# Kernel tuning notes

Hardware: AMD Instinct MI355X
Metric: run time of the kernel (lower is better)

The kernel has to match this reference:

```python
import jax, jax.numpy as jnp
import numpy as np


def setup_inputs() -> dict:
    key = jax.random.key(0)
    k1, k2 = jax.random.split(key)
    E, T, N = 65536, 4096, 10000
    edge_index = jax.random.randint(k1, (2, E), 0, N)
    # target edges are a subset of edge_index columns so every target exists
    target_edges = edge_index[:, :T]
    score = jax.random.normal(k2, (E,), dtype=jnp.float32)
    return {
        "edge_index": edge_index,
        "score": score,
        "target_edges": target_edges,
        "num_nodes": N,
    }


def reference(edge_index, score, target_edges, num_nodes):
    # Vectorized form of the per-target-edge loop:
    # for each target edge (s, d):
    #   mask_e      = (src_e == s) | (dst_e == d)
    #   CE over score[mask] with target = position of the exact edge (s, d)
    #   contribution = CE / K  where K = mask.sum()
    src, dst = edge_index[0], edge_index[1]            # [E]
    t_src, t_dst = target_edges[0], target_edges[1]    # [T]

    same_src = src[None, :] == t_src[:, None]          # [T, E]
    same_dst = dst[None, :] == t_dst[:, None]          # [T, E]
    mask = same_src | same_dst                         # candidate set per target
    is_tgt = same_src & same_dst                       # exact target edge hits

    exists = jnp.any(is_tgt, axis=1)                   # [T]
    K = jnp.sum(mask, axis=1).astype(score.dtype)      # [T] ragged subset sizes

    NEG = jnp.asarray(-1e30, score.dtype)
    masked_logits = jnp.where(mask, score[None, :], NEG)   # [T, E]
    lse = jax.nn.logsumexp(masked_logits, axis=1)           # [T]

    # argmax over bool picks the FIRST matching edge, matching torch argmax(-1)
    tgt_idx = jnp.argmax(is_tgt, axis=1)                # [T]
    tgt_logit = score[tgt_idx]                          # [T]

    # cross_entropy = lse - target_logit; divided by subset size K
    loss_t = jnp.where(exists, (lse - tgt_logit) / K, 0.0)
    return jnp.sum(loss_t) / target_edges.shape[1]
```

## Files before the change

### kernel.cpp

```cpp
#include <hip/hip_runtime.h>
#include <hip/hip_bf16.h>
#include <stdint.h>


#define HLOG 13
#define HSZ  (1u << HLOG)
#define NCAP 16384
#define EMPTY64 0xFFFFFFFFFFFFFFFFull
#define M40     ((1ull << 40) - 1)
#define CNT1    (1ull << 40)
#define FSCALE      4194304.0f
#define INV_FSCALE  (1.0f / 4194304.0f)

typedef unsigned long long u64;
typedef unsigned int u32;

__device__ __forceinline__ u32 hash64(u64 k) {
    return (u32)((k * 0x9E3779B97F4A7C15ull) >> (64 - HLOG));
}

__global__ __launch_bounds__(256) void la_insert(
    const int* __restrict__ tsrc, const int* __restrict__ tdst,
    u64* __restrict__ hkey, int T)
{
    const int t = blockIdx.x * 256 + threadIdx.x;
    if (t >= T) return;
    const u64 key = ((u64)(u32)tsrc[t] << 32) | (u32)tdst[t];
    u32 h = hash64(key);
    while (true) {
        const u64 prev = atomicCAS(&hkey[h], EMPTY64, key);
        if (prev == EMPTY64 || prev == key) break;
        h = (h + 1) & (HSZ - 1);
    }
}

__global__ __launch_bounds__(256) void la_edges(
    const int* __restrict__ src, const int* __restrict__ dst,
    const float* __restrict__ score,
    const u64* __restrict__ hkey, u64* __restrict__ hpack,
    u32* __restrict__ hmin,
    u64* __restrict__ nodeS, u64* __restrict__ nodeD, int E)
{
    const int e = blockIdx.x * 256 + threadIdx.x;
    if (e >= E) return;
    const int s = src[e], d = dst[e];
    const float ev = __expf(score[e]);
    const u64 add = (u64)(ev * FSCALE + 0.5f) + CNT1;

    atomicAdd(&nodeS[s], add);
    atomicAdd(&nodeD[d], add);

    const u64 key = ((u64)(u32)s << 32) | (u32)d;
    u32 h = hash64(key);
    while (true) {
        const u64 k2 = hkey[h];
        if (k2 == EMPTY64) break;
        if (k2 == key) {
            atomicAdd(&hpack[h], add);
            atomicMin(&hmin[h], (u32)e);
            break;
        }
        h = (h + 1) & (HSZ - 1);
    }
}

__global__ __launch_bounds__(64) void la_targets(
    const int* __restrict__ tsrc, const int* __restrict__ tdst,
    const float* __restrict__ score,
    const u64* __restrict__ hkey, const u64* __restrict__ hpack,
    const u32* __restrict__ hmin,
    const u64* __restrict__ nodeS, const u64* __restrict__ nodeD,
    float* __restrict__ partial, int T)
{
    const int t = blockIdx.x * 64 + threadIdx.x;
    float local = 0.0f;
    if (t < T) {
        const int a = tsrc[t], b = tdst[t];
        const u64 key = ((u64)(u32)a << 32) | (u32)b;
        u32 h = hash64(key);
        int slot = -1;
        while (true) {
            const u64 k2 = hkey[h];
            if (k2 == key) { slot = (int)h; break; }
            if (k2 == EMPTY64) break;
            h = (h + 1) & (HSZ - 1);
        }
        if (slot >= 0) {
            const u64 pk = hpack[slot];
            const u64 cb = pk >> 40;
            if (cb > 0) {
                const u64 pa = nodeS[a], pb = nodeD[b];
                const u64 Sfix = (pa & M40) + (pb & M40) - (pk & M40);
                const u64 Kc   = (pa >> 40) + (pb >> 40) - cb;
                const float S  = (float)Sfix * INV_FSCALE;
                local = (logf(S) - score[hmin[slot]]) / (float)Kc;
            }
        }
    }
    for (int off = 32; off > 0; off >>= 1) local += __shfl_down(local, off);
    if (threadIdx.x == 0) partial[blockIdx.x] = local;
}

__global__ __launch_bounds__(64) void la_final(
    const float* __restrict__ partial, float* __restrict__ out, int nb, int T)
{
    float s = 0.0f;
    for (int i = threadIdx.x; i < nb; i += 64) s += partial[i];
    for (int off = 32; off > 0; off >>= 1) s += __shfl_down(s, off);
    if (threadIdx.x == 0) out[0] = s / (float)T;
}

#define NT   8
#define BLK  256

__global__ __launch_bounds__(BLK) void la_loss_main(
    const int* __restrict__ src, const int* __restrict__ dst,
    const float* __restrict__ score,
    const int* __restrict__ tsrc, const int* __restrict__ tdst,
    float* __restrict__ partial, int E, int T)
{
    const int tid   = threadIdx.x;
    const int tbase = blockIdx.x * NT;
    if (tbase >= T) return;

    int ts[NT], td[NT];
#pragma unroll
    for (int j = 0; j < NT; ++j) {
        int tj = tbase + j; if (tj > T - 1) tj = T - 1;
        ts[j] = tsrc[tj];
        td[j] = tdst[tj];
    }

    float S[NT]; float Kc[NT]; int idx[NT];
#pragma unroll
    for (int j = 0; j < NT; ++j) { S[j] = 0.0f; Kc[j] = 0.0f; idx[j] = 0x7fffffff; }

    for (int it = tid * 4; it < E; it += BLK * 4) {
        const int4   vs = *reinterpret_cast<const int4*>(src + it);
        const int4   vd = *reinterpret_cast<const int4*>(dst + it);
        const float4 sc = *reinterpret_cast<const float4*>(score + it);
        const int   es[4] = { vs.x, vs.y, vs.z, vs.w };
        const int   ed[4] = { vd.x, vd.y, vd.z, vd.w };
        const float ev[4] = { __expf(sc.x), __expf(sc.y), __expf(sc.z), __expf(sc.w) };
#pragma unroll
        for (int j = 0; j < NT; ++j) {
#pragma unroll
            for (int k = 0; k < 4; ++k) {
                const bool ms = (es[k] == ts[j]);
                const bool md = (ed[k] == td[j]);
                const bool m  = ms | md;
                S[j]  += m ? ev[k] : 0.0f;
                Kc[j] += m ? 1.0f  : 0.0f;
                idx[j] = (ms & md) ? min(idx[j], it + k) : idx[j];
            }
        }
    }

#pragma unroll
    for (int j = 0; j < NT; ++j) {
        for (int off = 32; off > 0; off >>= 1) {
            S[j]  += __shfl_down(S[j],  off);
            Kc[j] += __shfl_down(Kc[j], off);
            idx[j] = min(idx[j], __shfl_down(idx[j], off));
        }
    }

    __shared__ float sS[4][NT];
    __shared__ float sK[4][NT];
    __shared__ int   sI[4][NT];
    const int wave = tid >> 6;
    const int lane = tid & 63;
    if (lane == 0) {
#pragma unroll
        for (int j = 0; j < NT; ++j) { sS[wave][j] = S[j]; sK[wave][j] = Kc[j]; sI[wave][j] = idx[j]; }
    }
    __syncthreads();

    if (tid < NT && (tbase + tid) < T) {
        float Ssum = 0.0f, Ksum = 0.0f;
        int im = 0x7fffffff;
#pragma unroll
        for (int w = 0; w < 4; ++w) {
            Ssum += sS[w][tid]; Ksum += sK[w][tid]; im = min(im, sI[w][tid]);
        }
        float loss = 0.0f;
        if (im != 0x7fffffff) loss = (logf(Ssum) - score[im]) / Ksum;
        partial[tbase + tid] = loss;
    }
}

__global__ __launch_bounds__(256) void la_loss_reduce(
    const float* __restrict__ partial, float* __restrict__ out, int T)
{
    float s = 0.0f;
    for (int i = threadIdx.x; i < T; i += 256) s += partial[i];
    for (int off = 32; off > 0; off >>= 1) s += __shfl_down(s, off);
    __shared__ float acc[4];
    if ((threadIdx.x & 63) == 0) acc[threadIdx.x >> 6] = s;
    __syncthreads();
    if (threadIdx.x == 0) out[0] = (acc[0] + acc[1] + acc[2] + acc[3]) / (float)T;
}


extern "C" void kernel_launch(void* const* d_in, const int* in_sizes, int n_in,
                              void* d_out, int out_size, void* d_ws, size_t ws_size,
                              hipStream_t stream) {
    const int*   edge_index = (const int*)d_in[0];
    const float* score      = (const float*)d_in[1];
    const int*   target     = (const int*)d_in[2];

    const int E = in_sizes[0] / 2;
    const int T = in_sizes[2] / 2;

    const int* src  = edge_index;
    const int* dst  = edge_index + E;
    const int* tsrc = target;
    const int* tdst = target + T;

    const size_t HKEY_B  = (size_t)HSZ * 8;
    const size_t HMIN_B  = (size_t)HSZ * 4;
    const size_t HPACK_B = (size_t)HSZ * 8;
    const size_t NODE_B  = (size_t)NCAP * 8;
    const int    nb3     = (T + 63) / 64;
    const size_t need = HKEY_B + HMIN_B + HPACK_B + 2 * NODE_B + (size_t)nb3 * 4;

    if (ws_size >= need) {
        uint8_t* p = (uint8_t*)d_ws;
        u64* hkey    = (u64*)p;                 p += HKEY_B;
        u32* hmin    = (u32*)p;                 p += HMIN_B;
        u64* hpack   = (u64*)p;                 p += HPACK_B;
        u64* nodeS   = (u64*)p;                 p += NODE_B;
        u64* nodeD   = (u64*)p;                 p += NODE_B;
        float* partial = (float*)p;

        hipMemsetAsync(hkey,  0xFF, HKEY_B + HMIN_B, stream);
        hipMemsetAsync(hpack, 0x00, HPACK_B + 2 * NODE_B, stream);

        la_insert<<<(T + 255) / 256, 256, 0, stream>>>(tsrc, tdst, hkey, T);
        la_edges<<<(E + 255) / 256, 256, 0, stream>>>(src, dst, score, hkey,
                                                      hpack, hmin, nodeS, nodeD, E);
        la_targets<<<nb3, 64, 0, stream>>>(tsrc, tdst, score, hkey, hpack, hmin,
                                           nodeS, nodeD, partial, T);
        la_final<<<1, 64, 0, stream>>>(partial, (float*)d_out, nb3, T);
    } else {
        float* partial = (float*)d_ws;
        la_loss_main<<<(T + NT - 1) / NT, BLK, 0, stream>>>(src, dst, score,
                                                            tsrc, tdst, partial, E, T);
        la_loss_reduce<<<1, 256, 0, stream>>>(partial, (float*)d_out, T);
    }
}
```

Before: 36.43 us.

## Filter edges by target-node bitmaps and fuse init and final reduction kernels

Replaces the two memsets with a single init kernel, and builds source/destination bitmaps of target nodes during hash insertion. The edge pass uses these bitmaps to skip atomics and hash probes for edges that touch no target node. The final reduction is folded into the targets kernel through a last-block-done counter with release/acquire atomics. This cuts launch count and atomic traffic, at the cost of extra bitmap atomics and a dependence on node ids being below NCAP.

```diff
diff --git a/kernel.cpp b/kernel.cpp
--- a/kernel.cpp
+++ b/kernel.cpp
@@ -6,6 +6,7 @@
 #define HLOG 13
 #define HSZ  (1u << HLOG)
 #define NCAP 16384
+#define NBW  (NCAP / 32)
 #define EMPTY64 0xFFFFFFFFFFFFFFFFull
 #define M40     ((1ull << 40) - 1)
 #define CNT1    (1ull << 40)
@@ -19,13 +20,29 @@
     return (u32)((k * 0x9E3779B97F4A7C15ull) >> (64 - HLOG));
 }
 
+#define FF_BYTES   ((size_t)HSZ * 8 + (size_t)HSZ * 4)
+#define Z_BYTES    ((size_t)HSZ * 8 + 2 * (size_t)NCAP * 8 + 2 * (size_t)NBW * 4 + 8)
+
+__global__ __launch_bounds__(256) void la_init(u64* __restrict__ p,
+                                               int n_ff, int n_tot)
+{
+    int i = blockIdx.x * 256 + threadIdx.x;
+    const int stride = gridDim.x * 256;
+    for (; i < n_tot; i += stride)
+        p[i] = (i < n_ff) ? EMPTY64 : 0ull;
+}
+
 __global__ __launch_bounds__(256) void la_insert(
     const int* __restrict__ tsrc, const int* __restrict__ tdst,
-    u64* __restrict__ hkey, int T)
+    u64* __restrict__ hkey, u32* __restrict__ sbit, u32* __restrict__ dbit,
+    int T)
 {
     const int t = blockIdx.x * 256 + threadIdx.x;
     if (t >= T) return;
-    const u64 key = ((u64)(u32)tsrc[t] << 32) | (u32)tdst[t];
+    const u32 a = (u32)tsrc[t], b = (u32)tdst[t];
+    if (a < NCAP) atomicOr(&sbit[a >> 5], 1u << (a & 31));
+    if (b < NCAP) atomicOr(&dbit[b >> 5], 1u << (b & 31));
+    const u64 key = ((u64)a << 32) | b;
     u32 h = hash64(key);
     while (true) {
         const u64 prev = atomicCAS(&hkey[h], EMPTY64, key);
@@ -39,28 +56,37 @@
     const float* __restrict__ score,
     const u64* __restrict__ hkey, u64* __restrict__ hpack,
     u32* __restrict__ hmin,
-    u64* __restrict__ nodeS, u64* __restrict__ nodeD, int E)
+    u64* __restrict__ nodeS, u64* __restrict__ nodeD,
+    const u32* __restrict__ sbit, const u32* __restrict__ dbit, int E)
 {
     const int e = blockIdx.x * 256 + threadIdx.x;
     if (e >= E) return;
-    const int s = src[e], d = dst[e];
+    const u32 s = (u32)src[e], d = (u32)dst[e];
+    if (s >= NCAP || d >= NCAP) return;
+
+    const bool hs = (sbit[s >> 5] >> (s & 31)) & 1u;
+    const bool hd = (dbit[d >> 5] >> (d & 31)) & 1u;
+    if (!hs && !hd) return;
+
     const float ev = __expf(score[e]);
     const u64 add = (u64)(ev * FSCALE + 0.5f) + CNT1;
 
-    atomicAdd(&nodeS[s], add);
-    atomicAdd(&nodeD[d], add);
-
-    const u64 key = ((u64)(u32)s << 32) | (u32)d;
-    u32 h = hash64(key);
-    while (true) {
-        const u64 k2 = hkey[h];
-        if (k2 == EMPTY64) break;
-        if (k2 == key) {
-            atomicAdd(&hpack[h], add);
-            atomicMin(&hmin[h], (u32)e);
-            break;
-        }
-        h = (h + 1) & (HSZ - 1);
+    if (hs) atomicAdd(&nodeS[s], add);
+    if (hd) atomicAdd(&nodeD[d], add);
+
+    if (hs && hd) {
+        const u64 key = ((u64)s << 32) | d;
+        u32 h = hash64(key);
+        while (true) {
+            const u64 k2 = hkey[h];
+            if (k2 == EMPTY64) break;
+            if (k2 == key) {
+                atomicAdd(&hpack[h], add);
+                atomicMin(&hmin[h], (u32)e);
+                break;
+            }
+            h = (h + 1) & (HSZ - 1);
+        }
     }
 }
 
@@ -70,13 +96,15 @@
     const u64* __restrict__ hkey, const u64* __restrict__ hpack,
     const u32* __restrict__ hmin,
     const u64* __restrict__ nodeS, const u64* __restrict__ nodeD,
-    float* __restrict__ partial, int T)
-{
-    const int t = blockIdx.x * 64 + threadIdx.x;
+    float* __restrict__ partial, u32* __restrict__ done,
+    float* __restrict__ out, int T)
+{
+    const int nb = gridDim.x;
+    const int t  = blockIdx.x * 64 + threadIdx.x;
     float local = 0.0f;
     if (t < T) {
-        const int a = tsrc[t], b = tdst[t];
-        const u64 key = ((u64)(u32)a << 32) | (u32)b;
+        const u32 a = (u32)tsrc[t], b = (u32)tdst[t];
+        const u64 key = ((u64)a << 32) | b;
         u32 h = hash64(key);
         int slot = -1;
         while (true) {
@@ -98,16 +126,25 @@
         }
     }
     for (int off = 32; off > 0; off >>= 1) local += __shfl_down(local, off);
-    if (threadIdx.x == 0) partial[blockIdx.x] = local;
-}
-
-__global__ __launch_bounds__(64) void la_final(
-    const float* __restrict__ partial, float* __restrict__ out, int nb, int T)
-{
-    float s = 0.0f;
-    for (int i = threadIdx.x; i < nb; i += 64) s += partial[i];
-    for (int off = 32; off > 0; off >>= 1) s += __shfl_down(s, off);
-    if (threadIdx.x == 0) out[0] = s / (float)T;
+
+    __shared__ int lastFlag;
+    if (threadIdx.x == 0) {
+        __hip_atomic_store(&partial[blockIdx.x], local, __ATOMIC_RELEASE,
+                           __HIP_MEMORY_SCOPE_AGENT);
+        const u32 prev = __hip_atomic_fetch_add(done, 1u, __ATOMIC_ACQ_REL,
+                                                __HIP_MEMORY_SCOPE_AGENT);
+        lastFlag = (prev == (u32)(nb - 1));
+    }
+    __syncthreads();
+
+    if (lastFlag) {
+        float s = 0.0f;
+        for (int i = threadIdx.x; i < nb; i += 64)
+            s += __hip_atomic_load(&partial[i], __ATOMIC_RELAXED,
+                                   __HIP_MEMORY_SCOPE_AGENT);
+        for (int off = 32; off > 0; off >>= 1) s += __shfl_down(s, off);
+        if (threadIdx.x == 0) out[0] = s / (float)T;
+    }
 }
 
 #define NT   8
@@ -217,31 +254,33 @@
     const int* tsrc = target;
     const int* tdst = target + T;
 
-    const size_t HKEY_B  = (size_t)HSZ * 8;
-    const size_t HMIN_B  = (size_t)HSZ * 4;
-    const size_t HPACK_B = (size_t)HSZ * 8;
-    const size_t NODE_B  = (size_t)NCAP * 8;
-    const int    nb3     = (T + 63) / 64;
-    const size_t need = HKEY_B + HMIN_B + HPACK_B + 2 * NODE_B + (size_t)nb3 * 4;
+    const int    nb   = (T + 63) / 64;
+    const size_t need = FF_BYTES + Z_BYTES + (size_t)nb * 4;
 
     if (ws_size >= need) {
         uint8_t* p = (uint8_t*)d_ws;
-        u64* hkey    = (u64*)p;                 p += HKEY_B;
-        u32* hmin    = (u32*)p;                 p += HMIN_B;
-        u64* hpack   = (u64*)p;                 p += HPACK_B;
-        u64* nodeS   = (u64*)p;                 p += NODE_B;
-        u64* nodeD   = (u64*)p;                 p += NODE_B;
+        u64* hkey  = (u64*)p;                          p += (size_t)HSZ * 8;
+        u32* hmin  = (u32*)p;                          p += (size_t)HSZ * 4;
+        u64* hpack = (u64*)p;                          p += (size_t)HSZ * 8;
+        u64* nodeS = (u64*)p;                          p += (size_t)NCAP * 8;
+        u64* nodeD = (u64*)p;                          p += (size_t)NCAP * 8;
+        u32* sbit  = (u32*)p;                          p += (size_t)NBW * 4;
+        u32* dbit  = (u32*)p;                          p += (size_t)NBW * 4;
+        u32* done  = (u32*)p;                          p += 8;
         float* partial = (float*)p;
 
-        hipMemsetAsync(hkey,  0xFF, HKEY_B + HMIN_B, stream);
-        hipMemsetAsync(hpack, 0x00, HPACK_B + 2 * NODE_B, stream);
-
-        la_insert<<<(T + 255) / 256, 256, 0, stream>>>(tsrc, tdst, hkey, T);
+        const int n_ff  = (int)(FF_BYTES / 8);
+        const int n_tot = (int)((FF_BYTES + Z_BYTES) / 8);
+
+        la_init<<<64, 256, 0, stream>>>((u64*)d_ws, n_ff, n_tot);
+        la_insert<<<(T + 255) / 256, 256, 0, stream>>>(tsrc, tdst, hkey,
+                                                       sbit, dbit, T);
         la_edges<<<(E + 255) / 256, 256, 0, stream>>>(src, dst, score, hkey,
-                                                      hpack, hmin, nodeS, nodeD, E);
-        la_targets<<<nb3, 64, 0, stream>>>(tsrc, tdst, score, hkey, hpack, hmin,
-                                           nodeS, nodeD, partial, T);
-        la_final<<<1, 64, 0, stream>>>(partial, (float*)d_out, nb3, T);
+                                                      hpack, hmin, nodeS, nodeD,
+                                                      sbit, dbit, E);
+        la_targets<<<nb, 64, 0, stream>>>(tsrc, tdst, score, hkey, hpack, hmin,
+                                          nodeS, nodeD, partial, done,
+                                          (float*)d_out, T);
     } else {
         float* partial = (float*)d_ws;
         la_loss_main<<<(T + NT - 1) / NT, BLK, 0, stream>>>(src, dst, score,
```

New measurement: 33.45 us. -8.2%, faster.
